# Kernel tuning notes

Measured on AMD Instinct MI355X. Metric: run time of the kernel, lower is better.

The kernel has to match this reference:

```python
import jax, jax.numpy as jnp
import numpy as np

D_MODEL = 1024
N_HEADS = 16


def setup_inputs() -> dict:
    key = jax.random.key(0)
    ks = jax.random.split(key, 7)
    s = 0.02
    x = jax.random.normal(ks[0], (4, 2048, D_MODEL), dtype=jnp.float32)
    Wq = jax.random.normal(ks[1], (D_MODEL, D_MODEL), dtype=jnp.float32) * s
    Wk = jax.random.normal(ks[2], (D_MODEL, D_MODEL), dtype=jnp.float32) * s
    Wv = jax.random.normal(ks[3], (D_MODEL, D_MODEL), dtype=jnp.float32) * s
    bq = jax.random.normal(ks[4], (D_MODEL,), dtype=jnp.float32) * s
    bk = jax.random.normal(ks[5], (D_MODEL,), dtype=jnp.float32) * s
    bv = jax.random.normal(ks[6], (D_MODEL,), dtype=jnp.float32) * s
    return {"x": x, "Wq": Wq, "bq": bq, "Wk": Wk, "bk": bk, "Wv": Wv, "bv": bv}


def reference(x, Wq, bq, Wk, bk, Wv, bv):
    B, S, D = x.shape
    H = N_HEADS
    hd = D // H
    # torch Linear: y = x @ W.T + b
    q = (x @ Wq.T + bq).reshape(B, S, H, hd).transpose(0, 2, 1, 3)  # [B,H,S,hd]
    k = (x @ Wk.T + bk).reshape(B, S, H, hd).transpose(0, 2, 1, 3)
    v = (x @ Wv.T + bv).reshape(B, S, H, hd).transpose(0, 2, 1, 3)
    # NOTE: source scales by sqrt(d_model), not sqrt(head_dim)
    scores = jnp.einsum('bhqd,bhkd->bhqk', q, k) / jnp.sqrt(jnp.float32(D))
    attn = jax.nn.softmax(scores, axis=-1)
    out = jnp.einsum('bhqk,bhkd->bhqd', attn, v)  # [B,H,S,hd]
    return out.transpose(0, 2, 1, 3).reshape(B, S, D)
```

## Files before the change

### kernel.cpp

```cpp
#include <hip/hip_runtime.h>
#include <hip/hip_bf16.h>

#define D_MODEL 1024
#define NHEADS  16
#define HD      64
#define BATCH   4
#define SEQ     2048

#define XELEMS (BATCH * SEQ * D_MODEL)
#define WELEMS (D_MODEL * D_MODEL)

#define PPITCH 72

typedef __attribute__((ext_vector_type(8))) short v8s;
typedef __attribute__((ext_vector_type(4))) float v4f;

using bf16 = __hip_bfloat16;

#define GLD_LDS(gp, lp) \
    __builtin_amdgcn_global_load_lds((const __attribute__((address_space(1))) void*)(gp), \
                                     (__attribute__((address_space(3))) void*)(lp), 16, 0, 0)

#if __has_builtin(__builtin_amdgcn_exp2f)
#define EXP2(x) __builtin_amdgcn_exp2f(x)
#else
#define EXP2(x) exp2f(x)
#endif

__device__ __forceinline__ unsigned int f2bf(float f) {
    union { float f; unsigned int u; } c; c.f = f;
    unsigned int u = c.u;
    u += 0x7fffu + ((u >> 16) & 1u);
    return u >> 16;
}

__device__ __forceinline__ unsigned int pack_bf16_hu(float lo, float hi) {
    unsigned int a = __float_as_uint(lo) + 0x8000u;
    unsigned int b = __float_as_uint(hi) + 0x8000u;
    return __builtin_amdgcn_perm(b, a, 0x07060302u);
}

__device__ __forceinline__ uint4 cvt8(const float* p) {
    float4 f0 = ((const float4*)p)[0];
    float4 f1 = ((const float4*)p)[1];
    uint4 r;
    r.x = f2bf(f0.x) | (f2bf(f0.y) << 16);
    r.y = f2bf(f0.z) | (f2bf(f0.w) << 16);
    r.z = f2bf(f1.x) | (f2bf(f1.y) << 16);
    r.w = f2bf(f1.z) | (f2bf(f1.w) << 16);
    return r;
}

__global__ void detect_dtype(const unsigned short* __restrict__ x16,
                             int* __restrict__ flag) {
    int lane = threadIdx.x;
    unsigned short v = x16[2 * lane];
    int e = (v >> 7) & 0xff;
    bool plaus = (e >= 90) && (e <= 141);
    unsigned long long m = __ballot(plaus);
    if (lane == 0) *flag = (__popcll(m) >= 48) ? 1 : 0;
}

__global__ __launch_bounds__(256) void convert_inputs(
    const void* __restrict__ x,
    const void* __restrict__ wq, const void* __restrict__ wk,
    const void* __restrict__ wv,
    const void* __restrict__ bq, const void* __restrict__ bk,
    const void* __restrict__ bv,
    bf16* __restrict__ xbf, bf16* __restrict__ wbf, bf16* __restrict__ bbf,
    const int* __restrict__ flag)
{
    const int isbf = *flag;
    long g = (long)blockIdx.x * 256 + threadIdx.x;
    const long xg = XELEMS / 8;
    const long wg = WELEMS / 8;
    const long bg = D_MODEL / 8;
    const void* src; bf16* dst; long off;
    if      (g < xg)                  { src = x;  dst = xbf;              off = g; }
    else if (g < xg + wg)             { src = wq; dst = wbf;              off = g - xg; }
    else if (g < xg + 2*wg)           { src = wk; dst = wbf + WELEMS;     off = g - xg - wg; }
    else if (g < xg + 3*wg)           { src = wv; dst = wbf + 2*WELEMS;   off = g - xg - 2*wg; }
    else if (g < xg + 3*wg + bg)      { src = bq; dst = bbf;              off = g - xg - 3*wg; }
    else if (g < xg + 3*wg + 2*bg)    { src = bk; dst = bbf + D_MODEL;    off = g - xg - 3*wg - bg; }
    else if (g < xg + 3*wg + 3*bg)    { src = bv; dst = bbf + 2*D_MODEL;  off = g - xg - 3*wg - 2*bg; }
    else return;
    uint4 r = isbf ? ((const uint4*)src)[off]
                   : cvt8((const float*)src + off * 8);
    ((uint4*)dst)[off] = r;
}

__global__ __launch_bounds__(256, 2) void qkv_gemm(
    const bf16* __restrict__ xbf, const bf16* __restrict__ wbf,
    const bf16* __restrict__ bbf,
    bf16* __restrict__ qout, bf16* __restrict__ kout, bf16* __restrict__ vout)
{
    __shared__ bf16 Atile[128 * 32];
    __shared__ bf16 Btile[128 * 32];

    const int z = blockIdx.z;
    const bf16* W    = wbf + (size_t)z * WELEMS;
    const bf16* bias = bbf + z * D_MODEL;
    bf16* out = (z == 0) ? qout : (z == 1) ? kout : vout;
    const float scale = (z == 0) ? (1.4426950408889634f / 32.0f) : 1.0f;

    const int tid  = threadIdx.x;
    const int lane = tid & 63;
    const int wave = tid >> 6;
    const int m0w  = (wave >> 1) * 64;
    const int n0w  = (wave & 1) * 64;
    const int m_base = blockIdx.x * 128;
    const int n_base = blockIdx.y * 128;

    const int lm   = lane & 15;
    const int quad = lane >> 4;
    const int lk   = quad * 8;

    v4f acc[4][4] = {};

    for (int k0 = 0; k0 < D_MODEL; k0 += 32) {
        __syncthreads();
        #pragma unroll
        for (int p = 0; p < 2; ++p) {
            int chunk = wave + 4 * p;
            int row   = chunk * 16 + (lane >> 2);
            const bf16* ga = xbf + (size_t)(m_base + row) * D_MODEL + k0 + (lane & 3) * 8;
            const bf16* gb = W   + (size_t)(n_base + row) * D_MODEL + k0 + (lane & 3) * 8;
            GLD_LDS(ga, Atile + chunk * 16 * 32);
            GLD_LDS(gb, Btile + chunk * 16 * 32);
        }
        __syncthreads();

        v8s afrag[4], bfrag[4];
        #pragma unroll
        for (int mt = 0; mt < 4; ++mt)
            afrag[mt] = *(const v8s*)(Atile + (m0w + mt * 16 + lm) * 32 + lk);
        #pragma unroll
        for (int nt = 0; nt < 4; ++nt)
            bfrag[nt] = *(const v8s*)(Btile + (n0w + nt * 16 + lm) * 32 + lk);
        #pragma unroll
        for (int mt = 0; mt < 4; ++mt)
            #pragma unroll
            for (int nt = 0; nt < 4; ++nt)
                acc[mt][nt] = __builtin_amdgcn_mfma_f32_16x16x32_bf16(
                    afrag[mt], bfrag[nt], acc[mt][nt], 0, 0, 0);
    }

    #pragma unroll
    for (int nt = 0; nt < 4; ++nt) {
        int n = n_base + n0w + nt * 16 + lm;
        float bb = __bfloat162float(bias[n]);
        int h = n >> 6, d = n & 63;
        #pragma unroll
        for (int mt = 0; mt < 4; ++mt) {
            if (z == 2) {
                int m = m_base + m0w + mt * 16 + quad * 4;
                int b = m >> 11, s = m & (SEQ - 1);
                float p0 = acc[mt][nt][0] + bb;
                float p1 = acc[mt][nt][1] + bb;
                float p2 = acc[mt][nt][2] + bb;
                float p3 = acc[mt][nt][3] + bb;
                uint2 pk;
                pk.x = pack_bf16_hu(p0, p1);
                pk.y = pack_bf16_hu(p2, p3);
                size_t bh = (size_t)(b * NHEADS + h);
                *(uint2*)(out + (((bh << 6) + d) << 11) + s) = pk;
            } else {
                #pragma unroll
                for (int r = 0; r < 4; ++r) {
                    int m = m_base + m0w + mt * 16 + quad * 4 + r;
                    int b = m >> 11, s = m & (SEQ - 1);
                    float vv = (acc[mt][nt][r] + bb) * scale;
                    size_t bh = (size_t)(b * NHEADS + h);
                    out[(((bh << 11) + s) << 6) + d] = __float2bfloat16(vv);
                }
            }
        }
    }
}

__global__ __launch_bounds__(256, 4) void attn(
    const bf16* __restrict__ q, const bf16* __restrict__ k,
    const bf16* __restrict__ vT, void* __restrict__ out,
    const int* __restrict__ flag)
{
    __shared__ bf16 Ks[8 * 512];
    __shared__ bf16 Vt[8 * 512];
    __shared__ bf16 Ps[128 * PPITCH];

    const int isbf = *flag;

    const int l   = blockIdx.x;
    const int idx = l >> 3;
    const int q0  = (idx & 15) * 128;
    const int bh  = (l & 7) + ((idx >> 4) << 3);
    const int b   = bh >> 4, h = bh & 15;
    const size_t head_base  = (size_t)bh * SEQ * HD;
    const size_t head_baseT = (size_t)bh * HD * SEQ;

    const int tid  = threadIdx.x;
    const int lane = tid & 63;
    const int wave = tid >> 6;
    const int lm   = lane & 15;
    const int quad = lane >> 4;

    const int slm = lane >> 2;
    const int sq  = lane & 3;
    const int fidx = (lm * 4 + quad) * 8;

    v8s aq[2][2];
    #pragma unroll
    for (int mt = 0; mt < 2; ++mt)
        #pragma unroll
        for (int kb = 0; kb < 2; ++kb)
            aq[mt][kb] = *(const v8s*)(q + head_base
                          + (size_t)(q0 + wave * 32 + mt * 16 + lm) * HD
                          + kb * 32 + quad * 8);

    float l_acc[2] = { 0.0f, 0.0f };
    v4f   O[2][4] = {};

    for (int kv0 = 0; kv0 < SEQ; kv0 += 64) {
        __syncthreads();
        #pragma unroll
        for (int j = 0; j < 2; ++j) {
            int c  = wave * 2 + j;
            int kt = c >> 1, kb = c & 1;
            const bf16* ga = k + head_base
                + (size_t)(kv0 + kt * 16 + slm) * HD + kb * 32 + sq * 8;
            GLD_LDS(ga, Ks + c * 512);
        }
        #pragma unroll
        for (int j = 0; j < 2; ++j) {
            int c  = wave * 2 + j;
            int kk = c >> 2, dt = c & 3;
            const bf16* gv = vT + head_baseT
                + (size_t)(dt * 16 + slm) * SEQ + kv0 + kk * 32 + sq * 8;
            GLD_LDS(gv, Vt + c * 512);
        }
        __syncthreads();

        v4f sc[4][2] = {};
        #pragma unroll
        for (int kb = 0; kb < 2; ++kb) {
            v8s kf[4];
            #pragma unroll
            for (int kt = 0; kt < 4; ++kt)
                kf[kt] = *(const v8s*)(Ks + (kt * 2 + kb) * 512 + fidx);
            #pragma unroll
            for (int kt = 0; kt < 4; ++kt)
                #pragma unroll
                for (int mt = 0; mt < 2; ++mt)
                    sc[kt][mt] = __builtin_amdgcn_mfma_f32_16x16x32_bf16(
                        kf[kt], aq[mt][kb], sc[kt][mt], 0, 0, 0);
        }

        #pragma unroll
        for (int mt = 0; mt < 2; ++mt) {
            #pragma unroll
            for (int kt = 0; kt < 4; ++kt) {
                float p0 = EXP2(sc[kt][mt][0]);
                float p1 = EXP2(sc[kt][mt][1]);
                float p2 = EXP2(sc[kt][mt][2]);
                float p3 = EXP2(sc[kt][mt][3]);
                l_acc[mt] += (p0 + p1) + (p2 + p3);
                uint2 pk;
                pk.x = pack_bf16_hu(p0, p1);
                pk.y = pack_bf16_hu(p2, p3);
                *(uint2*)(Ps + (wave * 32 + mt * 16 + lm) * PPITCH
                             + kt * 16 + quad * 4) = pk;
            }
        }

        #pragma unroll
        for (int kk = 0; kk < 2; ++kk) {
            v8s ap[2], bv8[4];
            #pragma unroll
            for (int mt = 0; mt < 2; ++mt)
                ap[mt] = *(const v8s*)(Ps + (wave * 32 + mt * 16 + lm) * PPITCH
                                          + kk * 32 + quad * 8);
            #pragma unroll
            for (int dt = 0; dt < 4; ++dt)
                bv8[dt] = *(const v8s*)(Vt + (kk * 4 + dt) * 512 + fidx);
            #pragma unroll
            for (int mt = 0; mt < 2; ++mt)
                #pragma unroll
                for (int dt = 0; dt < 4; ++dt)
                    O[mt][dt] = __builtin_amdgcn_mfma_f32_16x16x32_bf16(
                        ap[mt], bv8[dt], O[mt][dt], 0, 0, 0);
        }
    }

    float inv[2];
    #pragma unroll
    for (int mt = 0; mt < 2; ++mt) {
        float lsum = l_acc[mt];
        lsum += __shfl_xor(lsum, 16, 64);
        lsum += __shfl_xor(lsum, 32, 64);
        inv[mt] = 1.0f / lsum;
    }

    #pragma unroll
    for (int mt = 0; mt < 2; ++mt) {
        #pragma unroll
        for (int r = 0; r < 4; ++r) {
            float ir = __shfl(inv[mt], quad * 4 + r, 64);
            int s = q0 + wave * 32 + mt * 16 + quad * 4 + r;
            #pragma unroll
            for (int dt = 0; dt < 4; ++dt) {
                int d = dt * 16 + lm;
                size_t off = (size_t)(b * SEQ + s) * D_MODEL + h * HD + d;
                float val = O[mt][dt][r] * ir;
                if (isbf) ((bf16*)out)[off] = __float2bfloat16(val);
                else      ((float*)out)[off] = val;
            }
        }
    }
}

extern "C" void kernel_launch(void* const* d_in, const int* in_sizes, int n_in,
                              void* d_out, int out_size, void* d_ws, size_t ws_size,
                              hipStream_t stream) {
    const void* x  = d_in[0];
    const void* Wq = d_in[1];
    const void* bq = d_in[2];
    const void* Wk = d_in[3];
    const void* bk = d_in[4];
    const void* Wv = d_in[5];
    const void* bv = d_in[6];

    char* ws = (char*)d_ws;
    int*  flag = (int*)ws;
    bf16* wbf  = (bf16*)(ws + 256);
    bf16* bbf  = (bf16*)(ws + 256 + 3 * (size_t)WELEMS * 2);
    bf16* qws  = (bf16*)(ws + 256 + 3 * (size_t)WELEMS * 2 + 8192);
    const size_t per = (size_t)BATCH * NHEADS * SEQ * HD;
    bf16* kws = qws + per;
    bf16* vws = kws + per;

    bf16* xbf = (bf16*)d_out;

    detect_dtype<<<1, 64, 0, stream>>>((const unsigned short*)x, flag);

    const long ngroups = (long)XELEMS / 8 + 3L * (WELEMS / 8) + 3L * (D_MODEL / 8);
    convert_inputs<<<(int)((ngroups + 255) / 256), 256, 0, stream>>>(
        x, Wq, Wk, Wv, bq, bk, bv, xbf, wbf, bbf, flag);

    dim3 g1(64, 8, 3);
    qkv_gemm<<<g1, 256, 0, stream>>>(xbf, wbf, bbf, qws, kws, vws);

    attn<<<1024, 256, 0, stream>>>(qws, kws, vws, d_out, flag);
}
```

Measured before the change: 249.7 us.

## Keep softmax probabilities in registers via permlane swaps instead of LDS round-trip

The P tile used to be written to LDS and read back in the A-operand layout for the PV MFMA. It is now rearranged inside each wave's registers with permlane32/permlane16 swaps. The V-tile global-to-LDS load order is permuted so the key ordering matches the new register layout. This drops the LDS stores and loads for P and frees its shared memory, which could help occupancy. The cost is extra cross-lane permute instructions, and correctness depends on the K ordering matching the V layout exactly.

```diff
diff --git a/kernel.cpp b/kernel.cpp
--- a/kernel.cpp
+++ b/kernel.cpp
@@ -9,8 +9,6 @@
 
 #define XELEMS (BATCH * SEQ * D_MODEL)
 #define WELEMS (D_MODEL * D_MODEL)
-
-#define PPITCH 72
 
 typedef __attribute__((ext_vector_type(8))) short v8s;
 typedef __attribute__((ext_vector_type(4))) float v4f;
@@ -49,6 +47,27 @@
     r.z = f2bf(f1.x) | (f2bf(f1.y) << 16);
     r.w = f2bf(f1.z) | (f2bf(f1.w) << 16);
     return r;
+}
+
+__device__ __forceinline__ void qswap32(unsigned int &a, unsigned int &b) {
+#if __has_builtin(__builtin_amdgcn_permlane32_swap)
+    auto r = __builtin_amdgcn_permlane32_swap(a, b, false, false);
+    a = (unsigned int)r[0]; b = (unsigned int)r[1];
+#else
+    unsigned int ax = (unsigned int)__shfl_xor((int)a, 32, 64);
+    unsigned int bx = (unsigned int)__shfl_xor((int)b, 32, 64);
+    if (threadIdx.x & 32) { a = bx; } else { b = ax; }
+#endif
+}
+__device__ __forceinline__ void qswap16(unsigned int &a, unsigned int &b) {
+#if __has_builtin(__builtin_amdgcn_permlane16_swap)
+    auto r = __builtin_amdgcn_permlane16_swap(a, b, false, false);
+    a = (unsigned int)r[0]; b = (unsigned int)r[1];
+#else
+    unsigned int ax = (unsigned int)__shfl_xor((int)a, 16, 64);
+    unsigned int bx = (unsigned int)__shfl_xor((int)b, 16, 64);
+    if (threadIdx.x & 16) { a = bx; } else { b = ax; }
+#endif
 }
 
 __global__ void detect_dtype(const unsigned short* __restrict__ x16,
@@ -185,7 +204,6 @@
 {
     __shared__ bf16 Ks[8 * 512];
     __shared__ bf16 Vt[8 * 512];
-    __shared__ bf16 Ps[128 * PPITCH];
 
     const int isbf = *flag;
 
@@ -219,6 +237,8 @@
     float l_acc[2] = { 0.0f, 0.0f };
     v4f   O[2][4] = {};
 
+    typedef union { v8s v; unsigned int u[4]; } AB;
+
     for (int kv0 = 0; kv0 < SEQ; kv0 += 64) {
         __syncthreads();
         #pragma unroll
@@ -232,9 +252,9 @@
         #pragma unroll
         for (int j = 0; j < 2; ++j) {
             int c  = wave * 2 + j;
-            int kk = c >> 2, dt = c & 3;
+            int g1 = c >> 2, dt = c & 3;
             const bf16* gv = vT + head_baseT
-                + (size_t)(dt * 16 + slm) * SEQ + kv0 + kk * 32 + sq * 8;
+                + (size_t)(dt * 16 + slm) * SEQ + kv0 + sq * 16 + g1 * 8;
             GLD_LDS(gv, Vt + c * 512);
         }
         __syncthreads();
@@ -254,6 +274,7 @@
                         kf[kt], aq[mt][kb], sc[kt][mt], 0, 0, 0);
         }
 
+        unsigned int pw[2][4][2];
         #pragma unroll
         for (int mt = 0; mt < 2; ++mt) {
             #pragma unroll
@@ -263,30 +284,44 @@
                 float p2 = EXP2(sc[kt][mt][2]);
                 float p3 = EXP2(sc[kt][mt][3]);
                 l_acc[mt] += (p0 + p1) + (p2 + p3);
-                uint2 pk;
-                pk.x = pack_bf16_hu(p0, p1);
-                pk.y = pack_bf16_hu(p2, p3);
-                *(uint2*)(Ps + (wave * 32 + mt * 16 + lm) * PPITCH
-                             + kt * 16 + quad * 4) = pk;
+                pw[mt][kt][0] = pack_bf16_hu(p0, p1);
+                pw[mt][kt][1] = pack_bf16_hu(p2, p3);
             }
         }
 
         #pragma unroll
+        for (int mt = 0; mt < 2; ++mt)
+            #pragma unroll
+            for (int kt0 = 0; kt0 < 2; ++kt0)
+                #pragma unroll
+                for (int j = 0; j < 2; ++j)
+                    qswap32(pw[mt][kt0][j], pw[mt][kt0 + 2][j]);
+        #pragma unroll
+        for (int mt = 0; mt < 2; ++mt)
+            #pragma unroll
+            for (int g1 = 0; g1 < 2; ++g1)
+                #pragma unroll
+                for (int j = 0; j < 2; ++j)
+                    qswap16(pw[mt][2 * g1][j], pw[mt][2 * g1 + 1][j]);
+
+        #pragma unroll
         for (int kk = 0; kk < 2; ++kk) {
-            v8s ap[2], bv8[4];
-            #pragma unroll
-            for (int mt = 0; mt < 2; ++mt)
-                ap[mt] = *(const v8s*)(Ps + (wave * 32 + mt * 16 + lm) * PPITCH
-                                          + kk * 32 + quad * 8);
+            v8s bv8[4];
             #pragma unroll
             for (int dt = 0; dt < 4; ++dt)
                 bv8[dt] = *(const v8s*)(Vt + (kk * 4 + dt) * 512 + fidx);
             #pragma unroll
-            for (int mt = 0; mt < 2; ++mt)
+            for (int mt = 0; mt < 2; ++mt) {
+                AB a;
+                a.u[0] = pw[mt][2 * kk + 0][0];
+                a.u[1] = pw[mt][2 * kk + 0][1];
+                a.u[2] = pw[mt][2 * kk + 1][0];
+                a.u[3] = pw[mt][2 * kk + 1][1];
                 #pragma unroll
                 for (int dt = 0; dt < 4; ++dt)
                     O[mt][dt] = __builtin_amdgcn_mfma_f32_16x16x32_bf16(
-                        ap[mt], bv8[dt], O[mt][dt], 0, 0, 0);
+                        a.v, bv8[dt], O[mt][dt], 0, 0, 0);
+            }
         }
     }
 
```

Result: faster. 244.7 us (-2.0%).
